# Kernel tuning notes

Hardware: AMD Instinct MI355X
Metric: run time of the kernel (lower is better)

The kernel has to match this reference:

```python
import jax, jax.numpy as jnp
import numpy as np

A = 100.0
EPSILON = 0.1
NUM_NEG = 10
N = 100000
DIM = 64


def setup_inputs() -> dict:
    key = jax.random.key(0)
    k1, k2, k3 = jax.random.split(key, 3)
    x = jax.random.normal(k1, (N, DIM), dtype=jnp.float32)
    u_idx = jax.random.randint(k2, (N * NUM_NEG,), 0, N)
    v_idx = jax.random.randint(k3, (N * NUM_NEG,), 0, N)
    return {"x": x, "u_idx": u_idx, "v_idx": v_idx}


def reference(x, u_idx, v_idx):
    # Minkowski signature vector J = [-1, 1, ..., 1]
    J = jnp.ones((DIM,), dtype=x.dtype).at[0].set(-1.0)

    xu = x[u_idx]                      # (E, dim) gather
    xv = x[v_idx]                      # (E, dim) gather

    inner = jnp.sum(xu * xv * J, axis=-1)                 # (E,) Minkowski inner product
    inner = jnp.minimum(inner, -1.0 - 1e-7)               # clamp(max=-1-1e-7)
    dist = jnp.arccosh(-inner)                            # hyperbolic distance

    mask = dist < EPSILON                                 # data-dependent activity mask
    delta = jnp.where(mask, EPSILON - dist, 0.0)          # zero out inactive pairs

    energy = 0.5 * A * jnp.sum(delta ** 2) / NUM_NEG

    denom = jnp.sqrt(inner ** 2 - 1.0)
    force_mag = A * delta / NUM_NEG                       # already zero where inactive
    factor = jnp.where(mask, -(force_mag / (denom + 1e-9)), 0.0)[:, None]  # (E,1)

    grad = jnp.zeros_like(x)
    grad = grad.at[u_idx].add(factor * (xv * J))          # scatter-add over pairs
    grad = grad.at[v_idx].add(factor * (xu * J))
    return energy, grad
```

## Files before the change

kernel.cpp:

```cpp
#include <hip/hip_runtime.h>

#define EPS_F 0.1f
#define A_F 100.0f
#define NUMNEG_F 10.0f
#define EXP_EPS 1.1051709f
#define CAP 64
#define BATCH 16
#define NBLOCKS 4096

__global__ __launch_bounds__(256) void fill_kernel(
    const int* __restrict__ u_idx, const int* __restrict__ v_idx,
    int* __restrict__ counts, int* __restrict__ entries,
    float* __restrict__ out, int out_n, int E)
{
    const int tid = blockIdx.x * blockDim.x + threadIdx.x;
    const int nthreads = gridDim.x * blockDim.x;

    float4* o4 = (float4*)out;
    const int n4 = out_n >> 2;
    for (int i = tid; i < n4; i += nthreads) o4[i] = float4{0.f, 0.f, 0.f, 0.f};
    if (tid == 0)
        for (int i = n4 * 4; i < out_n; i++) out[i] = 0.f;

    for (int i = tid; i < E; i += nthreads) {
        const int u = u_idx[i];
        const int slot = atomicAdd(&counts[u], 1);
        if (slot < CAP) entries[u * CAP + slot] = v_idx[i];
    }
}

__device__ __forceinline__ float red2(float a, float b, int dist, bool sel) {
    const float fa = a + __shfl_xor(a, dist, 64);
    const float fb = b + __shfl_xor(b, dist, 64);
    return sel ? fb : fa;
}

__global__ __launch_bounds__(256) void node_kernel(
    const float* __restrict__ x,
    const int* __restrict__ counts,
    const int* __restrict__ entries,
    float* __restrict__ out,
    float* __restrict__ block_energy,
    int N)
{
    const int lane = threadIdx.x & 63;
    const int wib  = threadIdx.x >> 6;
    const int wave = (blockIdx.x * blockDim.x + threadIdx.x) >> 6;
    const int nwaves = (gridDim.x * blockDim.x) >> 6;
    const float sign = (lane == 0) ? -1.0f : 1.0f;
    float* __restrict__ grad = out + 1;

    const bool m32 = (lane & 32) != 0;
    const bool m16 = (lane & 16) != 0;
    const bool m8  = (lane & 8)  != 0;
    const bool m4  = (lane & 4)  != 0;
    const int  e4  = lane >> 2;

    float eacc = 0.0f;

    int u = wave;
    int deg = 0, myv = 0;
    if (u < N) {
        deg = counts[u];
        myv = entries[u * CAP + lane];
    }

    while (u < N) {
        const int deg_c = min(deg, CAP);
        const int myv_c = myv;
        const float xuj = x[(size_t)u * 64 + lane] * sign;

        const int un = u + nwaves;
        if (un < N) {
            deg = counts[un];
            myv = entries[un * CAP + lane];
        }

        float gacc = 0.0f;
        for (int k0 = 0; k0 < deg_c; k0 += BATCH) {
            const int bn = min(BATCH, deg_c - k0);

            int vs[BATCH]; float xv[BATCH], p[BATCH];
            #pragma unroll
            for (int k = 0; k < BATCH; k++) {
                if (k < bn) {
                    vs[k] = __builtin_amdgcn_readlane(myv_c, k0 + k);
                    xv[k] = x[(size_t)vs[k] * 64 + lane];
                    p[k]  = xuj * xv[k];
                } else { vs[k] = 0; xv[k] = 0.0f; p[k] = 0.0f; }
            }

            float q0 = red2(p[0], p[8],  32, m32);
            float q1 = red2(p[1], p[9],  32, m32);
            float q2 = red2(p[2], p[10], 32, m32);
            float q3 = red2(p[3], p[11], 32, m32);
            float q4 = red2(p[4], p[12], 32, m32);
            float q5 = red2(p[5], p[13], 32, m32);
            float q6 = red2(p[6], p[14], 32, m32);
            float q7 = red2(p[7], p[15], 32, m32);
            float r0 = red2(q0, q4, 16, m16);
            float r1 = red2(q1, q5, 16, m16);
            float r2 = red2(q2, q6, 16, m16);
            float r3 = red2(q3, q7, 16, m16);
            float s0 = red2(r0, r2, 8, m8);
            float s1 = red2(r1, r3, 8, m8);
            float t0 = red2(s0, s1, 4, m4);
            t0 += __shfl_xor(t0, 2, 64);
            t0 += __shfl_xor(t0, 1, 64);

            const float inner = fminf(t0, -1.0f - 1e-7f);
            const float s     = __builtin_amdgcn_sqrtf(fmaf(inner, inner, -1.0f));
            const float t     = s - inner;
            const bool  act   = (t < EXP_EPS) & (e4 < bn);
            const float dist  = __logf(t);
            const float delta = act ? (EPS_F - dist) : 0.0f;
            eacc = fmaf(delta, delta, eacc);
            const float factor = (-(A_F / NUMNEG_F)) * delta *
                                 __builtin_amdgcn_rcpf(s + 1e-9f);

            const unsigned long long ball = __ballot(act);
            #pragma unroll
            for (int k = 0; k < BATCH; k++) {
                if ((ball >> (4 * k)) & 1ull) {
                    const float fk = __uint_as_float(
                        __builtin_amdgcn_readlane(__float_as_uint(factor), 4 * k));
                    unsafeAtomicAdd(&grad[(size_t)vs[k] * 64 + lane], fk * xuj);
                    gacc = fmaf(fk, xv[k], gacc);
                }
            }
        }
        if (deg_c > 0)
            unsafeAtomicAdd(&grad[(size_t)u * 64 + lane], gacc * sign);
        u = un;
    }

    #pragma unroll
    for (int off = 32; off >= 1; off >>= 1) eacc += __shfl_xor(eacc, off, 64);
    __shared__ float se[4];
    if (lane == 0) se[wib] = eacc * 0.25f;
    __syncthreads();
    if (threadIdx.x == 0)
        block_energy[blockIdx.x] = se[0] + se[1] + se[2] + se[3];
}

__global__ __launch_bounds__(256) void energy_reduce_kernel(
    const float* __restrict__ block_energy, float* __restrict__ out, int n)
{
    const int lane = threadIdx.x & 63;
    const int wib  = threadIdx.x >> 6;
    float s = 0.0f;
    for (int i = threadIdx.x; i < n; i += 256) s += block_energy[i];
    #pragma unroll
    for (int off = 32; off >= 1; off >>= 1) s += __shfl_xor(s, off, 64);
    __shared__ float se[4];
    if (lane == 0) se[wib] = s;
    __syncthreads();
    if (threadIdx.x == 0)
        out[0] = (se[0] + se[1] + se[2] + se[3]) * (0.5f * A_F / NUMNEG_F);
}

extern "C" void kernel_launch(void* const* d_in, const int* in_sizes, int n_in,
                              void* d_out, int out_size, void* d_ws, size_t ws_size,
                              hipStream_t stream) {
    const float* x     = (const float*)d_in[0];
    const int*   u_idx = (const int*)d_in[1];
    const int*   v_idx = (const int*)d_in[2];
    float* out = (float*)d_out;
    const int E = in_sizes[1];
    const int N = in_sizes[0] / 64;

    char* ws = (char*)d_ws;
    int*   counts       = (int*)ws;
    int*   entries      = (int*)(ws + (1 << 20));
    float* block_energy = (float*)(ws + (1 << 20) + (size_t)N * CAP * 4 + (1 << 20));

    hipMemsetAsync(counts, 0, (size_t)N * sizeof(int), stream);

    fill_kernel<<<4096, 256, 0, stream>>>(u_idx, v_idx, counts, entries,
                                          out, out_size, E);

    node_kernel<<<NBLOCKS, 256, 0, stream>>>(x, counts, entries, out, block_energy, N);

    energy_reduce_kernel<<<1, 256, 0, stream>>>(block_energy, out, NBLOCKS);
}
```

Measured before the change: 323.5 us.

## Software-pipeline node gathers across two nodes and batch fill atomics

The node kernel now alternates between two nodes per wave, gathering the first batch of neighbour rows for the next node before computing the current one, so gather latency overlaps the reduction and atomic work. The fill kernel launches fewer blocks and issues four index loads and four atomics per thread up front, which gives more memory-level parallelism. The cost is higher register pressure from the doubled batch buffers, which may reduce occupancy, and more complex control flow.

```diff
diff --git a/kernel.cpp b/kernel.cpp
--- a/kernel.cpp
+++ b/kernel.cpp
@@ -7,6 +7,8 @@
 #define CAP 64
 #define BATCH 16
 #define NBLOCKS 4096
+#define FBLOCKS 1024
+#define FPER 4
 
 __global__ __launch_bounds__(256) void fill_kernel(
     const int* __restrict__ u_idx, const int* __restrict__ v_idx,
@@ -14,18 +16,33 @@
     float* __restrict__ out, int out_n, int E)
 {
     const int tid = blockIdx.x * blockDim.x + threadIdx.x;
-    const int nthreads = gridDim.x * blockDim.x;
+    const int nth = gridDim.x * blockDim.x;
 
     float4* o4 = (float4*)out;
     const int n4 = out_n >> 2;
-    for (int i = tid; i < n4; i += nthreads) o4[i] = float4{0.f, 0.f, 0.f, 0.f};
+    for (int i = tid; i < n4; i += nth) o4[i] = float4{0.f, 0.f, 0.f, 0.f};
     if (tid == 0)
         for (int i = n4 * 4; i < out_n; i++) out[i] = 0.f;
 
-    for (int i = tid; i < E; i += nthreads) {
+    int us[FPER], vv[FPER], sl[FPER];
+    #pragma unroll
+    for (int j = 0; j < FPER; j++) {
+        const int i = tid + j * nth;
+        us[j] = (i < E) ? u_idx[i] : -1;
+        vv[j] = (i < E) ? v_idx[i] : 0;
+    }
+    #pragma unroll
+    for (int j = 0; j < FPER; j++)
+        sl[j] = (us[j] >= 0) ? atomicAdd(&counts[us[j]], 1) : CAP;
+    #pragma unroll
+    for (int j = 0; j < FPER; j++)
+        if (us[j] >= 0 && sl[j] < CAP)
+            entries[(size_t)us[j] * CAP + sl[j]] = vv[j];
+
+    for (int i = tid + FPER * nth; i < E; i += nth) {
         const int u = u_idx[i];
-        const int slot = atomicAdd(&counts[u], 1);
-        if (slot < CAP) entries[u * CAP + slot] = v_idx[i];
+        const int s = atomicAdd(&counts[u], 1);
+        if (s < CAP) entries[(size_t)u * CAP + s] = v_idx[i];
     }
 }
 
@@ -58,80 +75,114 @@
 
     float eacc = 0.0f;
 
-    int u = wave;
-    int deg = 0, myv = 0;
-    if (u < N) {
-        deg = counts[u];
-        myv = entries[u * CAP + lane];
-    }
-
-    while (u < N) {
+    auto gather_batch = [&](int u, int deg, int myv, float& xuj,
+                            int (&vs)[BATCH], float (&xv)[BATCH]) -> int {
+        xuj = x[(size_t)u * 64 + lane] * sign;
+        const int bn = min(deg, BATCH);
+        #pragma unroll
+        for (int k = 0; k < BATCH; k++) {
+            if (k < bn) {
+                vs[k] = __builtin_amdgcn_readlane(myv, k);
+                xv[k] = x[(size_t)vs[k] * 64 + lane];
+            } else { vs[k] = 0; xv[k] = 0.0f; }
+        }
+        return bn;
+    };
+
+    auto process_batch = [&](float xuj, int (&vs)[BATCH], float (&xv)[BATCH],
+                             int bn, float& gacc) {
+        float p[BATCH];
+        #pragma unroll
+        for (int k = 0; k < BATCH; k++) p[k] = xuj * xv[k];
+
+        float q0 = red2(p[0], p[8],  32, m32);
+        float q1 = red2(p[1], p[9],  32, m32);
+        float q2 = red2(p[2], p[10], 32, m32);
+        float q3 = red2(p[3], p[11], 32, m32);
+        float q4 = red2(p[4], p[12], 32, m32);
+        float q5 = red2(p[5], p[13], 32, m32);
+        float q6 = red2(p[6], p[14], 32, m32);
+        float q7 = red2(p[7], p[15], 32, m32);
+        float r0 = red2(q0, q4, 16, m16);
+        float r1 = red2(q1, q5, 16, m16);
+        float r2 = red2(q2, q6, 16, m16);
+        float r3 = red2(q3, q7, 16, m16);
+        float s0 = red2(r0, r2, 8, m8);
+        float s1 = red2(r1, r3, 8, m8);
+        float t0 = red2(s0, s1, 4, m4);
+        t0 += __shfl_xor(t0, 2, 64);
+        t0 += __shfl_xor(t0, 1, 64);
+
+        const float inner = fminf(t0, -1.0f - 1e-7f);
+        const float s     = __builtin_amdgcn_sqrtf(fmaf(inner, inner, -1.0f));
+        const float t     = s - inner;
+        const bool  act   = (t < EXP_EPS) & (e4 < bn);
+        const float dist  = __logf(t);
+        const float delta = act ? (EPS_F - dist) : 0.0f;
+        eacc = fmaf(delta, delta, eacc);
+        const float factor = (-(A_F / NUMNEG_F)) * delta *
+                             __builtin_amdgcn_rcpf(s + 1e-9f);
+
+        const unsigned long long ball = __ballot(act);
+        #pragma unroll
+        for (int k = 0; k < BATCH; k++) {
+            if ((ball >> (4 * k)) & 1ull) {
+                const float fk = __uint_as_float(
+                    __builtin_amdgcn_readlane(__float_as_uint(factor), 4 * k));
+                unsafeAtomicAdd(&grad[(size_t)vs[k] * 64 + lane], fk * xuj);
+                gacc = fmaf(fk, xv[k], gacc);
+            }
+        }
+    };
+
+    auto compute_node = [&](int u, int deg, int myv, float xuj,
+                            int (&vs)[BATCH], float (&xv)[BATCH], int bn) {
+        float gacc = 0.0f;
+        process_batch(xuj, vs, xv, bn, gacc);
         const int deg_c = min(deg, CAP);
-        const int myv_c = myv;
-        const float xuj = x[(size_t)u * 64 + lane] * sign;
-
-        const int un = u + nwaves;
-        if (un < N) {
-            deg = counts[un];
-            myv = entries[un * CAP + lane];
-        }
-
-        float gacc = 0.0f;
-        for (int k0 = 0; k0 < deg_c; k0 += BATCH) {
-            const int bn = min(BATCH, deg_c - k0);
-
-            int vs[BATCH]; float xv[BATCH], p[BATCH];
+        for (int k0 = BATCH; k0 < deg_c; k0 += BATCH) {
+            const int bn2 = min(BATCH, deg_c - k0);
+            int vs2[BATCH]; float xv2[BATCH];
             #pragma unroll
             for (int k = 0; k < BATCH; k++) {
-                if (k < bn) {
-                    vs[k] = __builtin_amdgcn_readlane(myv_c, k0 + k);
-                    xv[k] = x[(size_t)vs[k] * 64 + lane];
-                    p[k]  = xuj * xv[k];
-                } else { vs[k] = 0; xv[k] = 0.0f; p[k] = 0.0f; }
+                if (k < bn2) {
+                    vs2[k] = __builtin_amdgcn_readlane(myv, k0 + k);
+                    xv2[k] = x[(size_t)vs2[k] * 64 + lane];
+                } else { vs2[k] = 0; xv2[k] = 0.0f; }
             }
-
-            float q0 = red2(p[0], p[8],  32, m32);
-            float q1 = red2(p[1], p[9],  32, m32);
-            float q2 = red2(p[2], p[10], 32, m32);
-            float q3 = red2(p[3], p[11], 32, m32);
-            float q4 = red2(p[4], p[12], 32, m32);
-            float q5 = red2(p[5], p[13], 32, m32);
-            float q6 = red2(p[6], p[14], 32, m32);
-            float q7 = red2(p[7], p[15], 32, m32);
-            float r0 = red2(q0, q4, 16, m16);
-            float r1 = red2(q1, q5, 16, m16);
-            float r2 = red2(q2, q6, 16, m16);
-            float r3 = red2(q3, q7, 16, m16);
-            float s0 = red2(r0, r2, 8, m8);
-            float s1 = red2(r1, r3, 8, m8);
-            float t0 = red2(s0, s1, 4, m4);
-            t0 += __shfl_xor(t0, 2, 64);
-            t0 += __shfl_xor(t0, 1, 64);
-
-            const float inner = fminf(t0, -1.0f - 1e-7f);
-            const float s     = __builtin_amdgcn_sqrtf(fmaf(inner, inner, -1.0f));
-            const float t     = s - inner;
-            const bool  act   = (t < EXP_EPS) & (e4 < bn);
-            const float dist  = __logf(t);
-            const float delta = act ? (EPS_F - dist) : 0.0f;
-            eacc = fmaf(delta, delta, eacc);
-            const float factor = (-(A_F / NUMNEG_F)) * delta *
-                                 __builtin_amdgcn_rcpf(s + 1e-9f);
-
-            const unsigned long long ball = __ballot(act);
-            #pragma unroll
-            for (int k = 0; k < BATCH; k++) {
-                if ((ball >> (4 * k)) & 1ull) {
-                    const float fk = __uint_as_float(
-                        __builtin_amdgcn_readlane(__float_as_uint(factor), 4 * k));
-                    unsafeAtomicAdd(&grad[(size_t)vs[k] * 64 + lane], fk * xuj);
-                    gacc = fmaf(fk, xv[k], gacc);
-                }
-            }
+            process_batch(xuj, vs2, xv2, bn2, gacc);
         }
         if (deg_c > 0)
             unsafeAtomicAdd(&grad[(size_t)u * 64 + lane], gacc * sign);
-        u = un;
+    };
+
+    int uA = wave, uB = wave + nwaves;
+    int degA = 0, myvA = 0, degB = 0, myvB = 0;
+    if (uA < N) { degA = counts[uA]; myvA = entries[(size_t)uA * CAP + lane]; }
+    if (uB < N) { degB = counts[uB]; myvB = entries[(size_t)uB * CAP + lane]; }
+
+    float xuA = 0.0f, xuB = 0.0f;
+    int vsA[BATCH], vsB[BATCH];
+    float xvA[BATCH], xvB[BATCH];
+    int bnA = 0, bnB = 0;
+
+    if (uA < N) bnA = gather_batch(uA, degA, myvA, xuA, vsA, xvA);
+
+    while (uA < N) {
+        if (uB < N) bnB = gather_batch(uB, degB, myvB, xuB, vsB, xvB);
+        const int uA2 = uA + 2 * nwaves;
+        int degA2 = 0, myvA2 = 0;
+        if (uA2 < N) { degA2 = counts[uA2]; myvA2 = entries[(size_t)uA2 * CAP + lane]; }
+        compute_node(uA, degA, myvA, xuA, vsA, xvA, bnA);
+        uA = uA2; degA = degA2; myvA = myvA2;
+
+        if (uB >= N) break;
+        if (uA < N) bnA = gather_batch(uA, degA, myvA, xuA, vsA, xvA);
+        const int uB2 = uB + 2 * nwaves;
+        int degB2 = 0, myvB2 = 0;
+        if (uB2 < N) { degB2 = counts[uB2]; myvB2 = entries[(size_t)uB2 * CAP + lane]; }
+        compute_node(uB, degB, myvB, xuB, vsB, xvB, bnB);
+        uB = uB2; degB = degB2; myvB = myvB2;
     }
 
     #pragma unroll
@@ -176,8 +227,8 @@
 
     hipMemsetAsync(counts, 0, (size_t)N * sizeof(int), stream);
 
-    fill_kernel<<<4096, 256, 0, stream>>>(u_idx, v_idx, counts, entries,
-                                          out, out_size, E);
+    fill_kernel<<<FBLOCKS, 256, 0, stream>>>(u_idx, v_idx, counts, entries,
+                                             out, out_size, E);
 
     node_kernel<<<NBLOCKS, 256, 0, stream>>>(x, counts, entries, out, block_energy, N);
 
```

Result: slower. 352.7 us (+9.0%).

## Build symmetric adjacency lists and drop scatter atomics in favor of owner-writes

Applied to the files above, without the earlier changes.

Each pair is now inserted into both endpoints' adjacency lists, so every node computes its full gradient from its own neighbors and writes it directly without atomics. This removes the scattered atomic adds to neighbor gradient rows and the zeroing of the grad buffer, and halves the energy scale because each pair is now counted twice. In exchange it doubles fill-phase atomics and entry writes, doubles the pairwise dot-product work and neighbor gathers, and raises per-node degree, which increases the chance of hitting the CAP=64 truncation.

```diff
diff --git a/kernel.cpp b/kernel.cpp
--- a/kernel.cpp
+++ b/kernel.cpp
@@ -11,21 +11,19 @@
 __global__ __launch_bounds__(256) void fill_kernel(
     const int* __restrict__ u_idx, const int* __restrict__ v_idx,
     int* __restrict__ counts, int* __restrict__ entries,
-    float* __restrict__ out, int out_n, int E)
+    float* __restrict__ out, int out_n, int grad_end, int E)
 {
     const int tid = blockIdx.x * blockDim.x + threadIdx.x;
-    const int nthreads = gridDim.x * blockDim.x;
+    const int nth = gridDim.x * blockDim.x;
 
-    float4* o4 = (float4*)out;
-    const int n4 = out_n >> 2;
-    for (int i = tid; i < n4; i += nthreads) o4[i] = float4{0.f, 0.f, 0.f, 0.f};
-    if (tid == 0)
-        for (int i = n4 * 4; i < out_n; i++) out[i] = 0.f;
+    for (int i = grad_end + tid; i < out_n; i += nth) out[i] = 0.f;
 
-    for (int i = tid; i < E; i += nthreads) {
-        const int u = u_idx[i];
-        const int slot = atomicAdd(&counts[u], 1);
-        if (slot < CAP) entries[u * CAP + slot] = v_idx[i];
+    for (int i = tid; i < E; i += nth) {
+        const int u = u_idx[i], v = v_idx[i];
+        const int s1 = atomicAdd(&counts[u], 1);
+        const int s2 = atomicAdd(&counts[v], 1);
+        if (s1 < CAP) entries[(size_t)u * CAP + s1] = v;
+        if (s2 < CAP) entries[(size_t)v * CAP + s2] = u;
     }
 }
 
@@ -62,7 +60,7 @@
     int deg = 0, myv = 0;
     if (u < N) {
         deg = counts[u];
-        myv = entries[u * CAP + lane];
+        myv = entries[(size_t)u * CAP + lane];
     }
 
     while (u < N) {
@@ -73,21 +71,21 @@
         const int un = u + nwaves;
         if (un < N) {
             deg = counts[un];
-            myv = entries[un * CAP + lane];
+            myv = entries[(size_t)un * CAP + lane];
         }
 
         float gacc = 0.0f;
         for (int k0 = 0; k0 < deg_c; k0 += BATCH) {
             const int bn = min(BATCH, deg_c - k0);
 
-            int vs[BATCH]; float xv[BATCH], p[BATCH];
+            float xv[BATCH], p[BATCH];
             #pragma unroll
             for (int k = 0; k < BATCH; k++) {
                 if (k < bn) {
-                    vs[k] = __builtin_amdgcn_readlane(myv_c, k0 + k);
-                    xv[k] = x[(size_t)vs[k] * 64 + lane];
+                    const int vk = __builtin_amdgcn_readlane(myv_c, k0 + k);
+                    xv[k] = x[(size_t)vk * 64 + lane];
                     p[k]  = xuj * xv[k];
-                } else { vs[k] = 0; xv[k] = 0.0f; p[k] = 0.0f; }
+                } else { xv[k] = 0.0f; p[k] = 0.0f; }
             }
 
             float q0 = red2(p[0], p[8],  32, m32);
@@ -124,20 +122,19 @@
                 if ((ball >> (4 * k)) & 1ull) {
                     const float fk = __uint_as_float(
                         __builtin_amdgcn_readlane(__float_as_uint(factor), 4 * k));
-                    unsafeAtomicAdd(&grad[(size_t)vs[k] * 64 + lane], fk * xuj);
                     gacc = fmaf(fk, xv[k], gacc);
                 }
             }
         }
-        if (deg_c > 0)
-            unsafeAtomicAdd(&grad[(size_t)u * 64 + lane], gacc * sign);
+
+        grad[(size_t)u * 64 + lane] = gacc * sign;
         u = un;
     }
 
     #pragma unroll
     for (int off = 32; off >= 1; off >>= 1) eacc += __shfl_xor(eacc, off, 64);
     __shared__ float se[4];
-    if (lane == 0) se[wib] = eacc * 0.25f;
+    if (lane == 0) se[wib] = eacc * 0.125f;
     __syncthreads();
     if (threadIdx.x == 0)
         block_energy[blockIdx.x] = se[0] + se[1] + se[2] + se[3];
@@ -177,7 +174,7 @@
     hipMemsetAsync(counts, 0, (size_t)N * sizeof(int), stream);
 
     fill_kernel<<<4096, 256, 0, stream>>>(u_idx, v_idx, counts, entries,
-                                          out, out_size, E);
+                                          out, out_size, 1 + N * 64, E);
 
     node_kernel<<<NBLOCKS, 256, 0, stream>>>(x, counts, entries, out, block_energy, N);
 
```

Measured after the change: 401.3 us. 1.24x slower.

## Shrink per-node bucket to 16 slots with overflow list and separate kernel

Applied to the files above, without the earlier changes.

Lowers the per-node adjacency capacity from 64 to 16 so each node is handled in one batch with no inner loop. Pairs beyond 16 per node go to a global overflow list, filled with an atomic counter and processed by a new edge-parallel kernel that scatters to both endpoints. This shrinks the entries buffer and removes loop overhead in the main kernel, and with mean degree about 10 most nodes fit in 16 slots. The cost is an extra kernel launch, a contended global atomic for overflow pairs, and a hard cap on overflow entries that silently drops pairs beyond it.

```diff
diff --git a/kernel.cpp b/kernel.cpp
--- a/kernel.cpp
+++ b/kernel.cpp
@@ -4,28 +4,37 @@
 #define A_F 100.0f
 #define NUMNEG_F 10.0f
 #define EXP_EPS 1.1051709f
-#define CAP 64
+#define CAP 16
 #define BATCH 16
 #define NBLOCKS 4096
+#define OVF_BLOCKS 128
+#define OVF_CAP (1 << 18)
 
 __global__ __launch_bounds__(256) void fill_kernel(
     const int* __restrict__ u_idx, const int* __restrict__ v_idx,
     int* __restrict__ counts, int* __restrict__ entries,
+    int* __restrict__ ovf_cnt, int* __restrict__ ovf_u, int* __restrict__ ovf_v,
     float* __restrict__ out, int out_n, int E)
 {
     const int tid = blockIdx.x * blockDim.x + threadIdx.x;
-    const int nthreads = gridDim.x * blockDim.x;
+    const int nth = gridDim.x * blockDim.x;
 
     float4* o4 = (float4*)out;
     const int n4 = out_n >> 2;
-    for (int i = tid; i < n4; i += nthreads) o4[i] = float4{0.f, 0.f, 0.f, 0.f};
+    for (int i = tid; i < n4; i += nth) o4[i] = float4{0.f, 0.f, 0.f, 0.f};
     if (tid == 0)
         for (int i = n4 * 4; i < out_n; i++) out[i] = 0.f;
 
-    for (int i = tid; i < E; i += nthreads) {
+    for (int i = tid; i < E; i += nth) {
         const int u = u_idx[i];
+        const int v = v_idx[i];
         const int slot = atomicAdd(&counts[u], 1);
-        if (slot < CAP) entries[u * CAP + slot] = v_idx[i];
+        if (slot < CAP) {
+            entries[u * CAP + slot] = v;
+        } else {
+            const int pos = atomicAdd(ovf_cnt, 1);
+            if (pos < OVF_CAP) { ovf_u[pos] = u; ovf_v[pos] = v; }
+        }
     }
 }
 
@@ -34,6 +43,35 @@
     const float fb = b + __shfl_xor(b, dist, 64);
     return sel ? fb : fa;
 }
+
+#define REDUCE_EPILOGUE(bn)                                                    \
+        float q0 = red2(p[0], p[8],  32, m32);                                 \
+        float q1 = red2(p[1], p[9],  32, m32);                                 \
+        float q2 = red2(p[2], p[10], 32, m32);                                 \
+        float q3 = red2(p[3], p[11], 32, m32);                                 \
+        float q4 = red2(p[4], p[12], 32, m32);                                 \
+        float q5 = red2(p[5], p[13], 32, m32);                                 \
+        float q6 = red2(p[6], p[14], 32, m32);                                 \
+        float q7 = red2(p[7], p[15], 32, m32);                                 \
+        float r0 = red2(q0, q4, 16, m16);                                      \
+        float r1 = red2(q1, q5, 16, m16);                                      \
+        float r2 = red2(q2, q6, 16, m16);                                      \
+        float r3 = red2(q3, q7, 16, m16);                                      \
+        float s0 = red2(r0, r2, 8, m8);                                        \
+        float s1 = red2(r1, r3, 8, m8);                                        \
+        float t0 = red2(s0, s1, 4, m4);                                        \
+        t0 += __shfl_xor(t0, 2, 64);                                           \
+        t0 += __shfl_xor(t0, 1, 64);                                           \
+        const float inner = fminf(t0, -1.0f - 1e-7f);                          \
+        const float sq    = __builtin_amdgcn_sqrtf(fmaf(inner, inner, -1.0f)); \
+        const float tt    = sq - inner;                                        \
+        const bool  act   = (tt < EXP_EPS) & (e4 < (bn));                      \
+        const float dist  = __logf(tt);                                        \
+        const float delta = act ? (EPS_F - dist) : 0.0f;                       \
+        eacc = fmaf(delta, delta, eacc);                                       \
+        const float factor = (-(A_F / NUMNEG_F)) * delta *                     \
+                             __builtin_amdgcn_rcpf(sq + 1e-9f);                \
+        const unsigned long long ball = __ballot(act)
 
 __global__ __launch_bounds__(256) void node_kernel(
     const float* __restrict__ x,
@@ -62,74 +100,43 @@
     int deg = 0, myv = 0;
     if (u < N) {
         deg = counts[u];
-        myv = entries[u * CAP + lane];
+        myv = entries[u * CAP + (lane & 15)];
     }
 
     while (u < N) {
-        const int deg_c = min(deg, CAP);
+        const int bn = min(deg, CAP);
         const int myv_c = myv;
         const float xuj = x[(size_t)u * 64 + lane] * sign;
 
         const int un = u + nwaves;
         if (un < N) {
             deg = counts[un];
-            myv = entries[un * CAP + lane];
-        }
+            myv = entries[un * CAP + (lane & 15)];
+        }
+
+        int vs[BATCH]; float xv[BATCH], p[BATCH];
+        #pragma unroll
+        for (int k = 0; k < BATCH; k++) {
+            if (k < bn) {
+                vs[k] = __builtin_amdgcn_readlane(myv_c, k);
+                xv[k] = x[(size_t)vs[k] * 64 + lane];
+                p[k]  = xuj * xv[k];
+            } else { vs[k] = 0; xv[k] = 0.0f; p[k] = 0.0f; }
+        }
+
+        REDUCE_EPILOGUE(bn);
 
         float gacc = 0.0f;
-        for (int k0 = 0; k0 < deg_c; k0 += BATCH) {
-            const int bn = min(BATCH, deg_c - k0);
-
-            int vs[BATCH]; float xv[BATCH], p[BATCH];
-            #pragma unroll
-            for (int k = 0; k < BATCH; k++) {
-                if (k < bn) {
-                    vs[k] = __builtin_amdgcn_readlane(myv_c, k0 + k);
-                    xv[k] = x[(size_t)vs[k] * 64 + lane];
-                    p[k]  = xuj * xv[k];
-                } else { vs[k] = 0; xv[k] = 0.0f; p[k] = 0.0f; }
+        #pragma unroll
+        for (int k = 0; k < BATCH; k++) {
+            if ((ball >> (4 * k)) & 1ull) {
+                const float fk = __uint_as_float(
+                    __builtin_amdgcn_readlane(__float_as_uint(factor), 4 * k));
+                unsafeAtomicAdd(&grad[(size_t)vs[k] * 64 + lane], fk * xuj);
+                gacc = fmaf(fk, xv[k], gacc);
             }
-
-            float q0 = red2(p[0], p[8],  32, m32);
-            float q1 = red2(p[1], p[9],  32, m32);
-            float q2 = red2(p[2], p[10], 32, m32);
-            float q3 = red2(p[3], p[11], 32, m32);
-            float q4 = red2(p[4], p[12], 32, m32);
-            float q5 = red2(p[5], p[13], 32, m32);
-            float q6 = red2(p[6], p[14], 32, m32);
-            float q7 = red2(p[7], p[15], 32, m32);
-            float r0 = red2(q0, q4, 16, m16);
-            float r1 = red2(q1, q5, 16, m16);
-            float r2 = red2(q2, q6, 16, m16);
-            float r3 = red2(q3, q7, 16, m16);
-            float s0 = red2(r0, r2, 8, m8);
-            float s1 = red2(r1, r3, 8, m8);
-            float t0 = red2(s0, s1, 4, m4);
-            t0 += __shfl_xor(t0, 2, 64);
-            t0 += __shfl_xor(t0, 1, 64);
-
-            const float inner = fminf(t0, -1.0f - 1e-7f);
-            const float s     = __builtin_amdgcn_sqrtf(fmaf(inner, inner, -1.0f));
-            const float t     = s - inner;
-            const bool  act   = (t < EXP_EPS) & (e4 < bn);
-            const float dist  = __logf(t);
-            const float delta = act ? (EPS_F - dist) : 0.0f;
-            eacc = fmaf(delta, delta, eacc);
-            const float factor = (-(A_F / NUMNEG_F)) * delta *
-                                 __builtin_amdgcn_rcpf(s + 1e-9f);
-
-            const unsigned long long ball = __ballot(act);
-            #pragma unroll
-            for (int k = 0; k < BATCH; k++) {
-                if ((ball >> (4 * k)) & 1ull) {
-                    const float fk = __uint_as_float(
-                        __builtin_amdgcn_readlane(__float_as_uint(factor), 4 * k));
-                    unsafeAtomicAdd(&grad[(size_t)vs[k] * 64 + lane], fk * xuj);
-                    gacc = fmaf(fk, xv[k], gacc);
-                }
-            }
-        }
-        if (deg_c > 0)
+        }
+        if (bn > 0)
             unsafeAtomicAdd(&grad[(size_t)u * 64 + lane], gacc * sign);
         u = un;
     }
@@ -141,6 +148,69 @@
     __syncthreads();
     if (threadIdx.x == 0)
         block_energy[blockIdx.x] = se[0] + se[1] + se[2] + se[3];
+}
+
+__global__ __launch_bounds__(256) void ovf_kernel(
+    const float* __restrict__ x,
+    const int* __restrict__ ovf_u, const int* __restrict__ ovf_v,
+    const int* __restrict__ ovf_cnt,
+    float* __restrict__ out, float* __restrict__ block_energy)
+{
+    const int lane = threadIdx.x & 63;
+    const int wib  = threadIdx.x >> 6;
+    const int wave = (blockIdx.x * blockDim.x + threadIdx.x) >> 6;
+    const int nwaves = (gridDim.x * blockDim.x) >> 6;
+    const float sign = (lane == 0) ? -1.0f : 1.0f;
+    float* __restrict__ grad = out + 1;
+
+    const bool m32 = (lane & 32) != 0;
+    const bool m16 = (lane & 16) != 0;
+    const bool m8  = (lane & 8)  != 0;
+    const bool m4  = (lane & 4)  != 0;
+    const int  e4  = lane >> 2;
+
+    const int nE = min(*ovf_cnt, OVF_CAP);
+    float eacc = 0.0f;
+
+    for (int base = wave * BATCH; base < nE; base += nwaves * BATCH) {
+        const int bn = min(BATCH, nE - base);
+
+        int uu = 0, vv = 0;
+        if (lane < bn) { uu = ovf_u[base + lane]; vv = ovf_v[base + lane]; }
+
+        int us[BATCH], vs[BATCH];
+        float xuj[BATCH], xv[BATCH], p[BATCH];
+        #pragma unroll
+        for (int k = 0; k < BATCH; k++) {
+            if (k < bn) {
+                us[k]  = __builtin_amdgcn_readlane(uu, k);
+                vs[k]  = __builtin_amdgcn_readlane(vv, k);
+                xuj[k] = x[(size_t)us[k] * 64 + lane] * sign;
+                xv[k]  = x[(size_t)vs[k] * 64 + lane];
+                p[k]   = xuj[k] * xv[k];
+            } else { us[k] = 0; vs[k] = 0; xuj[k] = 0.0f; xv[k] = 0.0f; p[k] = 0.0f; }
+        }
+
+        REDUCE_EPILOGUE(bn);
+
+        #pragma unroll
+        for (int k = 0; k < BATCH; k++) {
+            if ((ball >> (4 * k)) & 1ull) {
+                const float fk = __uint_as_float(
+                    __builtin_amdgcn_readlane(__float_as_uint(factor), 4 * k));
+                unsafeAtomicAdd(&grad[(size_t)vs[k] * 64 + lane], fk * xuj[k]);
+                unsafeAtomicAdd(&grad[(size_t)us[k] * 64 + lane], fk * xv[k] * sign);
+            }
+        }
+    }
+
+    #pragma unroll
+    for (int off = 32; off >= 1; off >>= 1) eacc += __shfl_xor(eacc, off, 64);
+    __shared__ float se[4];
+    if (lane == 0) se[wib] = eacc * 0.25f;
+    __syncthreads();
+    if (threadIdx.x == 0)
+        block_energy[NBLOCKS + blockIdx.x] = se[0] + se[1] + se[2] + se[3];
 }
 
 __global__ __launch_bounds__(256) void energy_reduce_kernel(
@@ -171,15 +241,21 @@
 
     char* ws = (char*)d_ws;
     int*   counts       = (int*)ws;
-    int*   entries      = (int*)(ws + (1 << 20));
-    float* block_energy = (float*)(ws + (1 << 20) + (size_t)N * CAP * 4 + (1 << 20));
-
-    hipMemsetAsync(counts, 0, (size_t)N * sizeof(int), stream);
+    int*   ovf_cnt      = (int*)(ws + (size_t)N * 4);
+    int*   entries      = (int*)(ws + (1u << 20));
+    int*   ovf_u        = (int*)(ws + (8u << 20));
+    int*   ovf_v        = (int*)(ws + (9u << 20));
+    float* block_energy = (float*)(ws + (10u << 20));
+
+    hipMemsetAsync(counts, 0, (size_t)(N + 1) * sizeof(int), stream);
 
     fill_kernel<<<4096, 256, 0, stream>>>(u_idx, v_idx, counts, entries,
+                                          ovf_cnt, ovf_u, ovf_v,
                                           out, out_size, E);
-
-    node_kernel<<<NBLOCKS, 256, 0, stream>>>(x, counts, entries, out, block_energy, N);
-
-    energy_reduce_kernel<<<1, 256, 0, stream>>>(block_energy, out, NBLOCKS);
-}
+    node_kernel<<<NBLOCKS, 256, 0, stream>>>(x, counts, entries, out,
+                                             block_energy, N);
+    ovf_kernel<<<OVF_BLOCKS, 256, 0, stream>>>(x, ovf_u, ovf_v, ovf_cnt,
+                                               out, block_energy);
+    energy_reduce_kernel<<<1, 256, 0, stream>>>(block_energy, out,
+                                                NBLOCKS + OVF_BLOCKS);
+}
```

Measured after the change: 352.6 us. 1.09x slower.
